# Optimization experiments

Hardware: AMD Instinct MI355X
Metric: run time of the kernel (lower is better)

The kernel has to match this reference:

```python
import jax, jax.numpy as jnp
import numpy as np

NEG_POS_RATIO = 3
B, N, C = 32, 32768, 21


def setup_inputs() -> dict:
    key = jax.random.key(0)
    k1, k2, k3, k4, k5 = jax.random.split(key, 5)
    confidence = jax.random.normal(k1, (B, N, C), dtype=jnp.float32)
    predicted_locations = jax.random.normal(k2, (B, N, 5), dtype=jnp.float32)
    gt_locations = jax.random.normal(k3, (B, N, 5), dtype=jnp.float32)
    raw = jax.random.randint(k4, (B, N), 1, C)
    is_pos = jax.random.uniform(k5, (B, N)) < 0.03
    labels = jnp.where(is_pos, raw, 0).astype(jnp.int32)
    return {
        "confidence": confidence,
        "predicted_locations": predicted_locations,
        "labels": labels,
        "gt_locations": gt_locations,
    }


def reference(confidence, predicted_locations, labels, gt_locations):
    # log-softmax over classes once; reused for mining and CE
    logp = jax.nn.log_softmax(confidence, axis=2)          # [B, N, C]

    # --- hard negative mining (no-grad in original) ---
    mining_loss = -jax.lax.stop_gradient(logp[:, :, 0])    # [B, N]
    pos_mask = labels > 0                                   # [B, N]
    num_pos = jnp.sum(pos_mask, axis=1, keepdims=True)      # [B, 1]
    num_neg = num_pos * NEG_POS_RATIO
    loss_m = jnp.where(pos_mask, -jnp.inf, mining_loss)
    idx = jnp.argsort(-loss_m, axis=1)      # descending sort indices
    orders = jnp.argsort(idx, axis=1)       # rank of each prior
    neg_mask = orders < num_neg
    mask = pos_mask | neg_mask

    # --- classification: summed CE over selected priors ---
    ce = -jnp.take_along_axis(logp, labels[..., None].astype(jnp.int32), axis=2)[..., 0]
    classification_loss = jnp.sum(jnp.where(mask, ce, 0.0))

    # --- localization: summed SmoothL1 over positive priors ---
    d = jnp.abs(predicted_locations - gt_locations)
    sl1 = jnp.where(d < 1.0, 0.5 * d * d, d - 0.5)
    smooth_l1_loss = jnp.sum(jnp.where(pos_mask[..., None], sl1, 0.0))

    n_pos = jnp.sum(pos_mask).astype(confidence.dtype)
    return (smooth_l1_loss / n_pos, classification_loss / n_pos)
```

## Files before the change

### kernel.cpp

```cpp
#include <hip/hip_runtime.h>
#include <cstdint>

#define BB 32
#define NN 32768
#define CC 21
#define K1_BLK 256
#define PPT 2
#define TILE (K1_BLK * PPT)
#define K1_GRID ((BB * NN) / TILE)
#define BLKROW (NN / TILE)

#define K2T 1024
#define NC 16

typedef float f4 __attribute__((ext_vector_type(4)));

__device__ __forceinline__ float fexp2(float x) {
    float r; asm("v_exp_f32 %0, %1" : "=v"(r) : "v"(x)); return r;
}
__device__ __forceinline__ float flog2(float x) {
    float r; asm("v_log_f32 %0, %1" : "=v"(r) : "v"(x)); return r;
}

__global__ __launch_bounds__(K1_BLK) void k1_compute(
    const float* __restrict__ conf, const float* __restrict__ pred,
    const int* __restrict__ labels, const float* __restrict__ gt,
    unsigned* __restrict__ keys, float* __restrict__ pce,
    float* __restrict__ psl1, int* __restrict__ pcnt,
    double* __restrict__ gsum, unsigned* __restrict__ done)
{
    __shared__ float wce[4], wsl[4];
    __shared__ int   wcnt[4];

    const int tid = threadIdx.x;
    const int lane = tid & 63;
    const int wid = tid >> 6;
    const size_t p0 = (size_t)blockIdx.x * TILE + tid;
    const size_t p1 = p0 + K1_BLK;

    if (blockIdx.x == 0 && tid == 0) { *done = 0u; *gsum = 0.0; }

    const int lab0 = labels[p0];
    const int lab1 = labels[p1];
    const float* cp0 = conf + p0 * CC;
    const float* cp1 = conf + p1 * CC;
    f4 A0, A1, A2, A3, A4, B0, B1, B2, B3, B4;
    __builtin_memcpy(&A0, cp0 +  0, 16);
    __builtin_memcpy(&A1, cp0 +  4, 16);
    __builtin_memcpy(&A2, cp0 +  8, 16);
    __builtin_memcpy(&A3, cp0 + 12, 16);
    __builtin_memcpy(&A4, cp0 + 16, 16);
    __builtin_memcpy(&B0, cp1 +  0, 16);
    __builtin_memcpy(&B1, cp1 +  4, 16);
    __builtin_memcpy(&B2, cp1 +  8, 16);
    __builtin_memcpy(&B3, cp1 + 12, 16);
    __builtin_memcpy(&B4, cp1 + 16, 16);
    const float a20 = cp0[20];
    const float b20 = cp1[20];

    const bool pos0 = lab0 > 0;
    const bool pos1 = lab1 > 0;

    float sl = 0.f;
    if (pos0) {
        const float* pp = pred + p0 * 5;
        const float* gg = gt + p0 * 5;
#pragma unroll
        for (int j = 0; j < 5; ++j) {
            float d = fabsf(pp[j] - gg[j]);
            sl += (d < 1.f) ? 0.5f * d * d : (d - 0.5f);
        }
    }
    if (pos1) {
        const float* pp = pred + p1 * 5;
        const float* gg = gt + p1 * 5;
#pragma unroll
        for (int j = 0; j < 5; ++j) {
            float d = fabsf(pp[j] - gg[j]);
            sl += (d < 1.f) ? 0.5f * d * d : (d - 0.5f);
        }
    }

    float s0 = 0.f, cl0 = 0.f;
#define KS(Q, J, IDX, LAB, SACC, CACC) { const float v_ = Q[J]; \
        SACC += fexp2(v_ * 1.44269504f); \
        CACC = ((IDX) == (LAB)) ? v_ : CACC; }
    KS(A0,0,0,lab0,s0,cl0) KS(A0,1,1,lab0,s0,cl0) KS(A0,2,2,lab0,s0,cl0) KS(A0,3,3,lab0,s0,cl0)
    KS(A1,0,4,lab0,s0,cl0) KS(A1,1,5,lab0,s0,cl0) KS(A1,2,6,lab0,s0,cl0) KS(A1,3,7,lab0,s0,cl0)
    KS(A2,0,8,lab0,s0,cl0) KS(A2,1,9,lab0,s0,cl0) KS(A2,2,10,lab0,s0,cl0) KS(A2,3,11,lab0,s0,cl0)
    KS(A3,0,12,lab0,s0,cl0) KS(A3,1,13,lab0,s0,cl0) KS(A3,2,14,lab0,s0,cl0) KS(A3,3,15,lab0,s0,cl0)
    KS(A4,0,16,lab0,s0,cl0) KS(A4,1,17,lab0,s0,cl0) KS(A4,2,18,lab0,s0,cl0) KS(A4,3,19,lab0,s0,cl0)
    { const float v_ = a20; s0 += fexp2(v_ * 1.44269504f); cl0 = (20 == lab0) ? v_ : cl0; }
    const float lse0 = 0.6931471805599453f * flog2(s0);
    const float mining0 = fmaxf(lse0 - A0[0], 0.f);
    keys[p0] = pos0 ? 0u : __float_as_uint(mining0);
    float ce = pos0 ? (lse0 - cl0) : 0.f;
    int cnt = pos0 ? 1 : 0;

    float s1 = 0.f, cl1 = 0.f;
    KS(B0,0,0,lab1,s1,cl1) KS(B0,1,1,lab1,s1,cl1) KS(B0,2,2,lab1,s1,cl1) KS(B0,3,3,lab1,s1,cl1)
    KS(B1,0,4,lab1,s1,cl1) KS(B1,1,5,lab1,s1,cl1) KS(B1,2,6,lab1,s1,cl1) KS(B1,3,7,lab1,s1,cl1)
    KS(B2,0,8,lab1,s1,cl1) KS(B2,1,9,lab1,s1,cl1) KS(B2,2,10,lab1,s1,cl1) KS(B2,3,11,lab1,s1,cl1)
    KS(B3,0,12,lab1,s1,cl1) KS(B3,1,13,lab1,s1,cl1) KS(B3,2,14,lab1,s1,cl1) KS(B3,3,15,lab1,s1,cl1)
    KS(B4,0,16,lab1,s1,cl1) KS(B4,1,17,lab1,s1,cl1) KS(B4,2,18,lab1,s1,cl1) KS(B4,3,19,lab1,s1,cl1)
    { const float v_ = b20; s1 += fexp2(v_ * 1.44269504f); cl1 = (20 == lab1) ? v_ : cl1; }
#undef KS
    const float lse1 = 0.6931471805599453f * flog2(s1);
    const float mining1 = fmaxf(lse1 - B0[0], 0.f);
    keys[p1] = pos1 ? 0u : __float_as_uint(mining1);
    ce += pos1 ? (lse1 - cl1) : 0.f;
    cnt += pos1 ? 1 : 0;

#pragma unroll
    for (int d = 32; d > 0; d >>= 1) {
        ce  += __shfl_down(ce, d);
        sl  += __shfl_down(sl, d);
        cnt += __shfl_down(cnt, d);
    }
    if (lane == 0) { wce[wid] = ce; wsl[wid] = sl; wcnt[wid] = cnt; }
    __syncthreads();
    if (tid == 0) {
        float tce = 0.f, tsl = 0.f; int tc = 0;
#pragma unroll
        for (int w = 0; w < 4; ++w) { tce += wce[w]; tsl += wsl[w]; tc += wcnt[w]; }
        pce[blockIdx.x]  = tce;
        psl1[blockIdx.x] = tsl;
        pcnt[blockIdx.x] = tc;
    }
}

template <class GET>
__device__ __forceinline__ void sscan2048(
    GET get, unsigned* ss, unsigned* swsum,
    int* s_bin, int* s_above, unsigned want, int tid, int lane, int wid)
{
    const int b0 = 2047 - 2 * tid;
    const int b1 = 2046 - 2 * tid;
    const unsigned m0 = get(b0), m1 = get(b1);
    unsigned v = m0 + m1;
#pragma unroll
    for (int d = 1; d < 64; d <<= 1) {
        unsigned u = __shfl_up(v, d);
        if (lane >= d) v += u;
    }
    if (lane == 63) swsum[wid] = v;
    __syncthreads();
    if (wid == 0) {
        unsigned wv = (lane < 16) ? swsum[lane] : 0;
#pragma unroll
        for (int d = 1; d < 16; d <<= 1) {
            unsigned u = __shfl_up(wv, d);
            if (lane >= d) wv += u;
        }
        if (lane < 16) swsum[lane] = wv;
    }
    __syncthreads();
    const unsigned off = wid ? swsum[wid - 1] : 0;
    const unsigned incl = off + v;
    const unsigned sb0 = incl - m1;
    ss[b0] = sb0;
    ss[b1] = incl;
    __syncthreads();
    if (sb0 >= want && (b0 == 2047 || ss[b0 + 1] < want)) {
        *s_bin = b0; *s_above = (b0 == 2047) ? 0 : (int)ss[b0 + 1];
    }
    if (incl >= want && ss[b1 + 1] < want) {
        *s_bin = b1; *s_above = (int)ss[b1 + 1];
    }
    __syncthreads();
}

__global__ __launch_bounds__(K2T, 8) void k2_select(
    const unsigned* __restrict__ keys, const int* __restrict__ pcnt,
    const float* __restrict__ pce, const float* __restrict__ psl1,
    double* __restrict__ gsum, unsigned* __restrict__ done,
    float* __restrict__ out)
{
    const int b = blockIdx.x;
    const int tid = threadIdx.x;
    const int lane = tid & 63;
    const int wid = tid >> 6;
    const unsigned* rk = keys + (size_t)b * NN;

    __shared__ unsigned h1[1024 * NC];
    __shared__ unsigned ss[2048];
    __shared__ unsigned swsum[16];
    __shared__ double sdA[16], sdB[16];
    __shared__ int sdI[16];
    __shared__ int s_bin, s_above, s_last;
    __shared__ unsigned s_want;

    uint4 kv[8];
    const uint4* rk4 = reinterpret_cast<const uint4*>(rk);
#pragma unroll
    for (int j = 0; j < 8; ++j) kv[j] = rk4[tid + j * K2T];

    if (wid == 0) {
        int c = pcnt[b * BLKROW + lane];
#pragma unroll
        for (int d = 32; d > 0; d >>= 1) c += __shfl_down(c, d);
        if (lane == 0) s_want = (unsigned)((3 * c > NN) ? NN : 3 * c);
    }
    for (int i = tid; i < 1024 * NC; i += K2T) h1[i] = 0;
    __syncthreads();
    const unsigned want = s_want;

    double rowval = 0.0;
    if (want > 0) {
        const unsigned cp = lane & (NC - 1);
#pragma unroll
        for (int j = 0; j < 8; ++j) {
            atomicAdd(&h1[((kv[j].x >> 21) << 4) | cp], 1u);
            atomicAdd(&h1[((kv[j].y >> 21) << 4) | cp], 1u);
            atomicAdd(&h1[((kv[j].z >> 21) << 4) | cp], 1u);
            atomicAdd(&h1[((kv[j].w >> 21) << 4) | cp], 1u);
        }
        __syncthreads();

        {
            const int bn = 1023 - tid;
            unsigned mv = 0;
#pragma unroll
            for (int c = 0; c < NC; ++c) mv += h1[(bn << 4) | c];
            unsigned v = mv;
#pragma unroll
            for (int d = 1; d < 64; d <<= 1) {
                unsigned u = __shfl_up(v, d);
                if (lane >= d) v += u;
            }
            if (lane == 63) swsum[wid] = v;
            __syncthreads();
            if (wid == 0) {
                unsigned wv = (lane < 16) ? swsum[lane] : 0;
#pragma unroll
                for (int d = 1; d < 16; d <<= 1) {
                    unsigned u = __shfl_up(wv, d);
                    if (lane >= d) wv += u;
                }
                if (lane < 16) swsum[lane] = wv;
            }
            __syncthreads();
            const unsigned incl = (wid ? swsum[wid - 1] : 0) + v;
            ss[bn] = incl;
            __syncthreads();
            if (incl >= want && (bn == 1023 || ss[bn + 1] < want)) {
                s_bin = bn; s_above = (bn == 1023) ? 0 : (int)ss[bn + 1];
            }
            __syncthreads();
        }
        const unsigned bsel1 = (unsigned)s_bin;
        const unsigned want1 = want - (unsigned)s_above;

        for (int i = tid; i < 4096; i += K2T) h1[i] = 0;
        __syncthreads();
        const unsigned c2 = lane & 1;
#pragma unroll
        for (int j = 0; j < 8; ++j) {
#define L2ADD(K) if (((K) >> 21) == bsel1) \
            atomicAdd(&h1[((((K) >> 10) & 0x7FFu) << 1) | c2], 1u);
            L2ADD(kv[j].x) L2ADD(kv[j].y) L2ADD(kv[j].z) L2ADD(kv[j].w)
#undef L2ADD
        }
        __syncthreads();
        sscan2048([&](int bn) { return h1[bn << 1] + h1[(bn << 1) | 1]; },
                  ss, swsum, &s_bin, &s_above, want1, tid, lane, wid);
        const unsigned bsel2 = (unsigned)s_bin;
        const unsigned want2 = want1 - (unsigned)s_above;
        const unsigned pref = (bsel1 << 11) | bsel2;

        double aboveS = 0.0, inS = 0.0;
        int inC = 0;
#pragma unroll
        for (int j = 0; j < 8; ++j) {
#define FIN(K) { const unsigned hp = (K) >> 10; \
            if (hp > pref) aboveS += (double)__uint_as_float(K); \
            else if (hp == pref) { inS += (double)__uint_as_float(K); inC++; } }
            FIN(kv[j].x) FIN(kv[j].y) FIN(kv[j].z) FIN(kv[j].w)
#undef FIN
        }
#pragma unroll
        for (int d = 32; d > 0; d >>= 1) {
            aboveS += __shfl_down(aboveS, d);
            inS    += __shfl_down(inS, d);
            inC    += __shfl_down(inC, d);
        }
        if (lane == 0) { sdA[wid] = aboveS; sdB[wid] = inS; sdI[wid] = inC; }
        __syncthreads();
        if (tid == 0) {
            double tA = 0.0, tB = 0.0; int tC = 0;
#pragma unroll
            for (int w = 0; w < 16; ++w) { tA += sdA[w]; tB += sdB[w]; tC += sdI[w]; }
            rowval = tA + tB * ((double)want2 / (double)tC);
        }
    }

    if (tid == 0) {
        const double oldv = atomicAdd(gsum, rowval);
        unsigned inc = (__double_as_longlong(oldv) == 0x7FF7DEADBEEF0123LL)
                           ? 2u : 1u;
        const unsigned old = atomicAdd(done, inc);
        s_last = (old == BB - 1) ? 1 : 0;
    }
    __syncthreads();

    if (s_last) {
        double ce = 0.0, sl = 0.0; int np = 0;
        for (int i = tid; i < K1_GRID; i += K2T) {
            ce += (double)pce[i];
            sl += (double)psl1[i];
            np += pcnt[i];
        }
#pragma unroll
        for (int d = 32; d > 0; d >>= 1) {
            ce += __shfl_down(ce, d);
            sl += __shfl_down(sl, d);
            np += __shfl_down(np, d);
        }
        if (lane == 0) { sdA[wid] = ce; sdB[wid] = sl; sdI[wid] = np; }
        __syncthreads();
        if (tid == 0) {
            double tce = 0.0, tsl = 0.0; int tnp = 0;
#pragma unroll
            for (int w = 0; w < 16; ++w) { tce += sdA[w]; tsl += sdB[w]; tnp += sdI[w]; }
            const double ns = atomicAdd(gsum, 0.0);
            const double npos = (double)tnp;
            out[0] = (float)(tsl / npos);
            out[1] = (float)((tce + ns) / npos);
        }
    }
}

extern "C" void kernel_launch(void* const* d_in, const int* in_sizes, int n_in,
                              void* d_out, int out_size, void* d_ws, size_t ws_size,
                              hipStream_t stream)
{
    const float* conf   = (const float*)d_in[0];
    const float* pred   = (const float*)d_in[1];
    const int*   labels = (const int*)d_in[2];
    const float* gt     = (const float*)d_in[3];
    float* out = (float*)d_out;

    char* ws = (char*)d_ws;
    unsigned* keys = (unsigned*)ws;
    float*    pce  = (float*)(ws + 4194304);
    float*    psl1 = (float*)(ws + 4202496);
    int*      pcnt = (int*)(ws + 4210688);
    double*   gsum = (double*)(ws + 4218880);
    unsigned* done = (unsigned*)(ws + 4218888);

    k1_compute<<<K1_GRID, K1_BLK, 0, stream>>>(conf, pred, labels, gt,
                                               keys, pce, psl1, pcnt,
                                               gsum, done);
    k2_select<<<BB, K2T, 0, stream>>>(keys, pcnt, pce, psl1,
                                      gsum, done, out);
}
```

Baseline: 37.51 us.

## Stage confidence rows into LDS via coalesced global_load_lds per wave

Each wave now copies its two 64-prior chunks of the confidence tensor into LDS with coalesced 16-byte global_load_lds transfers, instead of each thread doing strided per-row vector loads. The two halves are waited on separately, so the softmax for the first chunk can run while the second chunk is still loading. This aims to improve memory coalescing on the dominant input stream. In exchange it uses 48KB of LDS per block, which may limit occupancy, and per-thread LDS reads with stride 21 may cause bank conflicts.

```diff
diff --git a/kernel.cpp b/kernel.cpp
--- a/kernel.cpp
+++ b/kernel.cpp
@@ -9,11 +9,10 @@
 #define TILE (K1_BLK * PPT)
 #define K1_GRID ((BB * NN) / TILE)
 #define BLKROW (NN / TILE)
+#define WST 1536
 
 #define K2T 1024
 #define NC 16
-
-typedef float f4 __attribute__((ext_vector_type(4)));
 
 __device__ __forceinline__ float fexp2(float x) {
     float r; asm("v_exp_f32 %0, %1" : "=v"(r) : "v"(x)); return r;
@@ -29,37 +28,75 @@
     float* __restrict__ psl1, int* __restrict__ pcnt,
     double* __restrict__ gsum, unsigned* __restrict__ done)
 {
+    __shared__ __align__(16) float lconf[8 * WST];
     __shared__ float wce[4], wsl[4];
     __shared__ int   wcnt[4];
 
     const int tid = threadIdx.x;
     const int lane = tid & 63;
-    const int wid = tid >> 6;
-    const size_t p0 = (size_t)blockIdx.x * TILE + tid;
+    const int w = tid >> 6;
+    const int base = blockIdx.x * TILE;
+    const size_t p0 = (size_t)base + w * 64 + lane;
     const size_t p1 = p0 + K1_BLK;
 
     if (blockIdx.x == 0 && tid == 0) { *done = 0u; *gsum = 0.0; }
 
     const int lab0 = labels[p0];
     const int lab1 = labels[p1];
-    const float* cp0 = conf + p0 * CC;
-    const float* cp1 = conf + p1 * CC;
-    f4 A0, A1, A2, A3, A4, B0, B1, B2, B3, B4;
-    __builtin_memcpy(&A0, cp0 +  0, 16);
-    __builtin_memcpy(&A1, cp0 +  4, 16);
-    __builtin_memcpy(&A2, cp0 +  8, 16);
-    __builtin_memcpy(&A3, cp0 + 12, 16);
-    __builtin_memcpy(&A4, cp0 + 16, 16);
-    __builtin_memcpy(&B0, cp1 +  0, 16);
-    __builtin_memcpy(&B1, cp1 +  4, 16);
-    __builtin_memcpy(&B2, cp1 +  8, 16);
-    __builtin_memcpy(&B3, cp1 + 12, 16);
-    __builtin_memcpy(&B4, cp1 + 16, 16);
-    const float a20 = cp0[20];
-    const float b20 = cp1[20];
+
+    float* l0 = lconf + (w * 2 + 0) * WST;
+    float* l1 = lconf + (w * 2 + 1) * WST;
+    const char* g0 = (const char*)(conf + (size_t)(base + w * 64) * CC);
+    const char* g1 = (const char*)(conf + (size_t)(base + K1_BLK + w * 64) * CC);
+#pragma unroll
+    for (int s = 0; s < 6; ++s) {
+        int slot = s * 64 + lane;
+        if (s == 5) slot = (slot > 335) ? 335 : slot;
+        __builtin_amdgcn_global_load_lds(
+            (const __attribute__((address_space(1))) unsigned*)(g0 + (size_t)slot * 16),
+            (__attribute__((address_space(3))) unsigned*)(l0 + s * 256), 16, 0, 0);
+    }
+#pragma unroll
+    for (int s = 0; s < 6; ++s) {
+        int slot = s * 64 + lane;
+        if (s == 5) slot = (slot > 335) ? 335 : slot;
+        __builtin_amdgcn_global_load_lds(
+            (const __attribute__((address_space(1))) unsigned*)(g1 + (size_t)slot * 16),
+            (__attribute__((address_space(3))) unsigned*)(l1 + s * 256), 16, 0, 0);
+    }
 
     const bool pos0 = lab0 > 0;
     const bool pos1 = lab1 > 0;
+
+    asm volatile("s_waitcnt vmcnt(6)" ::: "memory");
+    __builtin_amdgcn_sched_barrier(0);
+
+    const float* my0 = l0 + lane * CC;
+    float s0 = 0.f;
+#pragma unroll
+    for (int c = 0; c < CC; ++c) s0 += fexp2(my0[c] * 1.44269504f);
+    const float lse0 = 0.6931471805599453f * flog2(s0);
+    const float c00 = my0[0];
+    const float cl0 = my0[lab0];
+    const float mining0 = fmaxf(lse0 - c00, 0.f);
+    keys[p0] = pos0 ? 0u : __float_as_uint(mining0);
+    float ce = pos0 ? (lse0 - cl0) : 0.f;
+    int cnt = pos0 ? 1 : 0;
+
+    asm volatile("s_waitcnt vmcnt(0)" ::: "memory");
+    __builtin_amdgcn_sched_barrier(0);
+
+    const float* my1 = l1 + lane * CC;
+    float s1 = 0.f;
+#pragma unroll
+    for (int c = 0; c < CC; ++c) s1 += fexp2(my1[c] * 1.44269504f);
+    const float lse1 = 0.6931471805599453f * flog2(s1);
+    const float c10 = my1[0];
+    const float cl1 = my1[lab1];
+    const float mining1 = fmaxf(lse1 - c10, 0.f);
+    keys[p1] = pos1 ? 0u : __float_as_uint(mining1);
+    ce += pos1 ? (lse1 - cl1) : 0.f;
+    cnt += pos1 ? 1 : 0;
 
     float sl = 0.f;
     if (pos0) {
@@ -81,48 +118,18 @@
         }
     }
 
-    float s0 = 0.f, cl0 = 0.f;
-#define KS(Q, J, IDX, LAB, SACC, CACC) { const float v_ = Q[J]; \
-        SACC += fexp2(v_ * 1.44269504f); \
-        CACC = ((IDX) == (LAB)) ? v_ : CACC; }
-    KS(A0,0,0,lab0,s0,cl0) KS(A0,1,1,lab0,s0,cl0) KS(A0,2,2,lab0,s0,cl0) KS(A0,3,3,lab0,s0,cl0)
-    KS(A1,0,4,lab0,s0,cl0) KS(A1,1,5,lab0,s0,cl0) KS(A1,2,6,lab0,s0,cl0) KS(A1,3,7,lab0,s0,cl0)
-    KS(A2,0,8,lab0,s0,cl0) KS(A2,1,9,lab0,s0,cl0) KS(A2,2,10,lab0,s0,cl0) KS(A2,3,11,lab0,s0,cl0)
-    KS(A3,0,12,lab0,s0,cl0) KS(A3,1,13,lab0,s0,cl0) KS(A3,2,14,lab0,s0,cl0) KS(A3,3,15,lab0,s0,cl0)
-    KS(A4,0,16,lab0,s0,cl0) KS(A4,1,17,lab0,s0,cl0) KS(A4,2,18,lab0,s0,cl0) KS(A4,3,19,lab0,s0,cl0)
-    { const float v_ = a20; s0 += fexp2(v_ * 1.44269504f); cl0 = (20 == lab0) ? v_ : cl0; }
-    const float lse0 = 0.6931471805599453f * flog2(s0);
-    const float mining0 = fmaxf(lse0 - A0[0], 0.f);
-    keys[p0] = pos0 ? 0u : __float_as_uint(mining0);
-    float ce = pos0 ? (lse0 - cl0) : 0.f;
-    int cnt = pos0 ? 1 : 0;
-
-    float s1 = 0.f, cl1 = 0.f;
-    KS(B0,0,0,lab1,s1,cl1) KS(B0,1,1,lab1,s1,cl1) KS(B0,2,2,lab1,s1,cl1) KS(B0,3,3,lab1,s1,cl1)
-    KS(B1,0,4,lab1,s1,cl1) KS(B1,1,5,lab1,s1,cl1) KS(B1,2,6,lab1,s1,cl1) KS(B1,3,7,lab1,s1,cl1)
-    KS(B2,0,8,lab1,s1,cl1) KS(B2,1,9,lab1,s1,cl1) KS(B2,2,10,lab1,s1,cl1) KS(B2,3,11,lab1,s1,cl1)
-    KS(B3,0,12,lab1,s1,cl1) KS(B3,1,13,lab1,s1,cl1) KS(B3,2,14,lab1,s1,cl1) KS(B3,3,15,lab1,s1,cl1)
-    KS(B4,0,16,lab1,s1,cl1) KS(B4,1,17,lab1,s1,cl1) KS(B4,2,18,lab1,s1,cl1) KS(B4,3,19,lab1,s1,cl1)
-    { const float v_ = b20; s1 += fexp2(v_ * 1.44269504f); cl1 = (20 == lab1) ? v_ : cl1; }
-#undef KS
-    const float lse1 = 0.6931471805599453f * flog2(s1);
-    const float mining1 = fmaxf(lse1 - B0[0], 0.f);
-    keys[p1] = pos1 ? 0u : __float_as_uint(mining1);
-    ce += pos1 ? (lse1 - cl1) : 0.f;
-    cnt += pos1 ? 1 : 0;
-
 #pragma unroll
     for (int d = 32; d > 0; d >>= 1) {
         ce  += __shfl_down(ce, d);
         sl  += __shfl_down(sl, d);
         cnt += __shfl_down(cnt, d);
     }
-    if (lane == 0) { wce[wid] = ce; wsl[wid] = sl; wcnt[wid] = cnt; }
+    if (lane == 0) { wce[w] = ce; wsl[w] = sl; wcnt[w] = cnt; }
     __syncthreads();
     if (tid == 0) {
         float tce = 0.f, tsl = 0.f; int tc = 0;
 #pragma unroll
-        for (int w = 0; w < 4; ++w) { tce += wce[w]; tsl += wsl[w]; tc += wcnt[w]; }
+        for (int v = 0; v < 4; ++v) { tce += wce[v]; tsl += wsl[v]; tc += wcnt[v]; }
         pce[blockIdx.x]  = tce;
         psl1[blockIdx.x] = tsl;
         pcnt[blockIdx.x] = tc;
```

New measurement: 39.64 us. 1.06x slower.
